# Kernel optimization log

Hardware: AMD Instinct MI355X
Metric: run time of the kernel (lower is better)

Reference implementation:

```python
import jax, jax.numpy as jnp
import numpy as np

N_HEADS = 16
ROPE_BASE = 10000.0


def _rope(x):
    # x: (B, T, H, D) -> rotary position embedding, half-split style
    T, D = x.shape[1], x.shape[-1]
    inv_freq = 1.0 / (ROPE_BASE ** (jnp.arange(0, D, 2, dtype=jnp.float32) / D))  # (D/2,)
    ang = jnp.arange(T, dtype=jnp.float32)[:, None] * inv_freq[None, :]            # (T, D/2)
    cos = jnp.cos(ang)[None, :, None, :].astype(x.dtype)
    sin = jnp.sin(ang)[None, :, None, :].astype(x.dtype)
    x1, x2 = jnp.split(x, 2, axis=-1)
    return jnp.concatenate([x1 * cos - x2 * sin, x2 * cos + x1 * sin], axis=-1)


def setup_inputs() -> dict:
    key = jax.random.key(0)
    k1, k2, k3 = jax.random.split(key, 3)
    B, T, C = 4, 2048, 2048
    init_std = 0.02
    n_layers = 24  # n_text_layers + n_vision_layers
    x = jax.random.normal(k1, (B, T, C), dtype=jnp.float32)
    Wqkv = jax.random.normal(k2, (C, 3 * C), dtype=jnp.float32) * init_std
    Wproj = jax.random.normal(k3, (C, C), dtype=jnp.float32) * (init_std * 2 * n_layers ** (-0.5))
    return {"x": x, "Wqkv": Wqkv, "Wproj": Wproj}


def reference(x, Wqkv, Wproj):
    B, T, C = x.shape
    D = C // N_HEADS
    qkv = x @ Wqkv                                  # (B, T, 3C) fused QKV projection
    q, k, v = jnp.split(qkv, 3, axis=-1)
    q = q.reshape(B, T, N_HEADS, D)
    k = k.reshape(B, T, N_HEADS, D)
    v = v.reshape(B, T, N_HEADS, D)
    q = _rope(q)
    k = _rope(k)
    y = jax.nn.dot_product_attention(q, k, v, is_causal=True)  # (B, T, H, D)
    y = y.reshape(B, T, C)
    return y @ Wproj
```

## Files before the change

### kernel.cpp

```cpp
#include <hip/hip_runtime.h>

#define BB 4
#define TT 2048
#define CC 2048
#define NHEAD 16
#define DH 128
#define MM (BB * TT)
#define N3 (3 * CC)
#define LD3 6144

typedef unsigned short u16;
typedef __attribute__((ext_vector_type(8))) short short8;
typedef __attribute__((ext_vector_type(4))) float f32x4;

__device__ __forceinline__ u16 f2bf(float f) {
  unsigned u = __float_as_uint(f);
  u += 0x7fffu + ((u >> 16) & 1u);
  return (u16)(u >> 16);
}
__device__ __forceinline__ float bf2f(u16 h) {
  return __uint_as_float(((unsigned)h) << 16);
}

__device__ __forceinline__ void gload_lds16(const void* g, void* l) {
  __builtin_amdgcn_global_load_lds((const __attribute__((address_space(1))) void*)g,
                                   (__attribute__((address_space(3))) void*)l, 16, 0, 0);
}

__device__ __forceinline__ f32x4 mfma16(short8 a, short8 b, f32x4 c) {
  return __builtin_amdgcn_mfma_f32_16x16x32_bf16(a, b, c, 0, 0, 0);
}

__global__ void convert_x_kernel(const float* __restrict__ x, u16* __restrict__ xb) {
  const int total = (MM * CC) / 4;
  const float4* xv = (const float4*)x;
  ushort4* ov = (ushort4*)xb;
  for (int i = blockIdx.x * blockDim.x + threadIdx.x; i < total; i += gridDim.x * blockDim.x) {
    float4 v = xv[i];
    ushort4 o;
    o.x = f2bf(v.x); o.y = f2bf(v.y); o.z = f2bf(v.z); o.w = f2bf(v.w);
    ov[i] = o;
  }
}

__global__ void transpose_bf16_kernel(const float* __restrict__ W, u16* __restrict__ Wt,
                                      int rows, int cols) {
  __shared__ float tile[32][33];
  const int n0 = blockIdx.x * 32, k0 = blockIdx.y * 32;
  const int tx = threadIdx.x, ty = threadIdx.y;
  #pragma unroll
  for (int i = 0; i < 4; ++i)
    tile[ty + 8 * i][tx] = W[(size_t)(k0 + ty + 8 * i) * cols + n0 + tx];
  __syncthreads();
  #pragma unroll
  for (int i = 0; i < 4; ++i)
    Wt[(size_t)(n0 + ty + 8 * i) * rows + k0 + tx] = f2bf(tile[tx][ty + 8 * i]);
}

__global__ void rope_table_kernel(float2* __restrict__ tab) {
  int idx = blockIdx.x * 256 + threadIdx.x;
  int t = idx >> 6, f = idx & 63;
  float freq = expf(-0.14391156831f * (float)f);
  float ang = (float)t * freq;
  float s, c;
  sincosf(ang, &s, &c);
  tab[idx] = make_float2(c, s);
}

__global__ void rope_apply_kernel(u16* __restrict__ qkv, const float2* __restrict__ tab) {
  int idx = blockIdx.x * 256 + threadIdx.x;
  int f8 = idx & 7;
  int h = (idx >> 3) & 15;
  int m = (idx >> 7) & 8191;
  int which = idx >> 20;
  int t = m & (TT - 1);
  u16* p = qkv + (size_t)m * LD3 + which * CC + h * DH + f8 * 8;
  short8 v1 = *(const short8*)p;
  short8 v2 = *(const short8*)(p + 64);
  const float2* cs = &tab[(t << 6) + f8 * 8];
  const float scale = which ? 1.0f : 0.08838834764831845f;
  short8 o1, o2;
  #pragma unroll
  for (int j = 0; j < 8; ++j) {
    float2 c = cs[j];
    float x1 = bf2f((u16)v1[j]), x2 = bf2f((u16)v2[j]);
    o1[j] = (short)f2bf((x1 * c.x - x2 * c.y) * scale);
    o2[j] = (short)f2bf((x2 * c.x + x1 * c.y) * scale);
  }
  *(short8*)p = o1;
  *(short8*)(p + 64) = o2;
}

#define TILE_B 32768

__device__ __forceinline__ int swz47(int x) { return x ^ (((x >> 7) & 7) << 4); }

__device__ __forceinline__ void stage_chunk(const u16* __restrict__ src, int K, int k0,
                                            char* ldsTile, int kind, int wid, int lane) {
  #pragma unroll
  for (int c = 0; c < 2; ++c) {
    int x;
    if (kind < 2) {
      x = (kind ? 8192 : 0) + c * 16384 + wid * 1024 + lane * 16;
    } else {
      int wl = wid * 2 + c;
      x = ((kind == 3) ? 4096 : 0) + (wl >> 2) * 8192 + (wl & 3) * 1024 + lane * 16;
    }
    int l = swz47(x);
    int r = l >> 7;
    int ce = (l >> 1) & 63;
    gload_lds16(src + (size_t)r * K + k0 + ce, ldsTile + (x - lane * 16));
  }
}

__global__ __launch_bounds__(512, 2) void gemm_bt_256(const u16* __restrict__ A,
                                                      const u16* __restrict__ Bt,
                                                      void* __restrict__ Cout,
                                                      int K, int ldc, int out_bf16) {
  __shared__ __align__(16) char As[2][TILE_B];
  __shared__ __align__(16) char Bs[2][TILE_B];
  const int tid = threadIdx.x;
  const int wid = tid >> 6, lane = tid & 63;
  const int l15 = lane & 15, g = lane >> 4;
  const int wr = wid >> 2, wc = wid & 3;
  const int nwg = gridDim.x * gridDim.y;
  const int orig = blockIdx.y * gridDim.x + blockIdx.x;
  const int swz = (orig & 7) * (nwg >> 3) + (orig >> 3);
  const int bx = swz % gridDim.x, by = swz / gridDim.x;
  const int row0 = by * 256, col0 = bx * 256;

  const u16* Ab = A + (size_t)row0 * K;
  const u16* Bb = Bt + (size_t)col0 * K;

  f32x4 acc[8][4];
  #pragma unroll
  for (int m = 0; m < 8; ++m)
    #pragma unroll
    for (int n = 0; n < 4; ++n) acc[m][n] = (f32x4){0.f, 0.f, 0.f, 0.f};

  const int abase = (wr * 128 + l15) * 128 + g * 16;
  const int bbase = (wc * 64 + l15) * 128 + g * 16;

  stage_chunk(Ab, K, 0, As[0], 0, wid, lane);
  stage_chunk(Bb, K, 0, Bs[0], 2, wid, lane);
  stage_chunk(Ab, K, 0, As[0], 1, wid, lane);
  stage_chunk(Bb, K, 0, Bs[0], 3, wid, lane);
  asm volatile("s_waitcnt vmcnt(0)" ::: "memory");
  __builtin_amdgcn_s_barrier();

  const int nt = K >> 6;
  short8 a[4][2], b[4][2];
  for (int t = 0; t < nt; ++t) {
    const int cur = t & 1, nxt = cur ^ 1;
    const bool hn = (t + 1) < nt;
    const int kn = (t + 1) << 6;
    const char* At = As[cur];
    const char* Btile = Bs[cur];

    if (hn) {
      stage_chunk(Ab, K, kn, As[nxt], 0, wid, lane);
      stage_chunk(Bb, K, kn, Bs[nxt], 2, wid, lane);
    }
    #pragma unroll
    for (int m = 0; m < 4; ++m)
      #pragma unroll
      for (int ks = 0; ks < 2; ++ks)
        a[m][ks] = *(const short8*)(At + swz47(abase + m * 2048 + ks * 64));
    #pragma unroll
    for (int n = 0; n < 2; ++n)
      #pragma unroll
      for (int ks = 0; ks < 2; ++ks)
        b[n][ks] = *(const short8*)(Btile + swz47(bbase + n * 2048 + ks * 64));
    __builtin_amdgcn_s_setprio(1);
    #pragma unroll
    for (int m = 0; m < 4; ++m)
      #pragma unroll
      for (int n = 0; n < 2; ++n)
        #pragma unroll
        for (int ks = 0; ks < 2; ++ks)
          acc[m][n] = mfma16(a[m][ks], b[n][ks], acc[m][n]);
    __builtin_amdgcn_s_setprio(0);

    if (hn) {
      stage_chunk(Ab, K, kn, As[nxt], 1, wid, lane);
      stage_chunk(Bb, K, kn, Bs[nxt], 3, wid, lane);
    }
    if (hn) asm volatile("s_waitcnt vmcnt(8)" ::: "memory");
    else    asm volatile("s_waitcnt vmcnt(0)" ::: "memory");
    __builtin_amdgcn_s_barrier();

    #pragma unroll
    for (int n = 2; n < 4; ++n)
      #pragma unroll
      for (int ks = 0; ks < 2; ++ks)
        b[n][ks] = *(const short8*)(Btile + swz47(bbase + n * 2048 + ks * 64));
    __builtin_amdgcn_s_setprio(1);
    #pragma unroll
    for (int m = 0; m < 4; ++m)
      #pragma unroll
      for (int n = 2; n < 4; ++n)
        #pragma unroll
        for (int ks = 0; ks < 2; ++ks)
          acc[m][n] = mfma16(a[m][ks], b[n][ks], acc[m][n]);
    __builtin_amdgcn_s_setprio(0);

    #pragma unroll
    for (int m = 0; m < 4; ++m)
      #pragma unroll
      for (int ks = 0; ks < 2; ++ks)
        a[m][ks] = *(const short8*)(At + swz47(abase + (m + 4) * 2048 + ks * 64));
    __builtin_amdgcn_s_setprio(1);
    #pragma unroll
    for (int m = 0; m < 4; ++m)
      #pragma unroll
      for (int n = 0; n < 2; ++n)
        #pragma unroll
        for (int ks = 0; ks < 2; ++ks)
          acc[m + 4][n] = mfma16(a[m][ks], b[n][ks], acc[m + 4][n]);
    __builtin_amdgcn_s_setprio(0);

    __builtin_amdgcn_s_setprio(1);
    #pragma unroll
    for (int m = 0; m < 4; ++m)
      #pragma unroll
      for (int n = 2; n < 4; ++n)
        #pragma unroll
        for (int ks = 0; ks < 2; ++ks)
          acc[m + 4][n] = mfma16(a[m][ks], b[n][ks], acc[m + 4][n]);
    __builtin_amdgcn_s_setprio(0);

    if (hn) {
      asm volatile("s_waitcnt vmcnt(4)" ::: "memory");
      __builtin_amdgcn_s_barrier();
    }
  }

  if (out_bf16) {
    u16* Cb = (u16*)Cout;
    #pragma unroll
    for (int m = 0; m < 8; ++m)
      #pragma unroll
      for (int n = 0; n < 4; ++n) {
        int row = row0 + wr * 128 + m * 16 + 4 * g;
        int col = col0 + wc * 64 + n * 16 + l15;
        #pragma unroll
        for (int j = 0; j < 4; ++j)
          Cb[(size_t)(row + j) * ldc + col] = f2bf(acc[m][n][j]);
      }
  } else {
    float* Cf = (float*)Cout;
    #pragma unroll
    for (int m = 0; m < 8; ++m)
      #pragma unroll
      for (int n = 0; n < 4; ++n) {
        int row = row0 + wr * 128 + m * 16 + 4 * g;
        int col = col0 + wc * 64 + n * 16 + l15;
        #pragma unroll
        for (int j = 0; j < 4; ++j)
          Cf[(size_t)(row + j) * ldc + col] = acc[m][n][j];
      }
  }
}

#define QBLK 128
#define KBLK 64
#define PADV 72

__global__ __launch_bounds__(256, 2) void attn_kernel(const u16* __restrict__ qkv,
                                                      u16* __restrict__ y) {
  __shared__ __align__(16) u16 Ks[2][KBLK * 128];
  __shared__ __align__(16) u16 Vt[2][DH * PADV];
  const int tid = threadIdx.x;
  const int wid = tid >> 6, lane = tid & 63;
  const int l15 = lane & 15, g = lane >> 4;
  const int b = blockIdx.y >> 4, h = blockIdx.y & 15;
  const size_t rb = (size_t)b * TT;
  const int vk0 = (tid & 15) * 4, vd0 = (tid >> 4) * 8;

  for (int half = 0; half < 2; ++half) {
    const int qt0 = (half ? (15 - (int)blockIdx.x) : (int)blockIdx.x) * QBLK;

    short8 qf[2][4];
    {
      const u16* qbase = qkv + (rb + qt0 + wid * 32 + l15) * LD3 + h * DH;
      #pragma unroll
      for (int f = 0; f < 2; ++f)
        #pragma unroll
        for (int kk = 0; kk < 4; ++kk)
          qf[f][kk] = *(const short8*)(qbase + f * 16 * LD3 + kk * 32 + g * 8);
    }

    {
      const u16* kbase = qkv + (rb)*LD3 + CC + h * DH;
      #pragma unroll
      for (int c = 0; c < 4; ++c) {
        int chunk = c * 256 + tid;
        int r = chunk >> 4, s = chunk & 15;
        gload_lds16(kbase + (size_t)r * LD3 + (size_t)((s ^ (r & 7)) * 8),
                    &Ks[0][(c * 256 + wid * 64) * 8]);
      }
      const u16* vg = qkv + (rb + vk0) * LD3 + 2 * CC + h * DH + vd0;
      short8 r0 = *(const short8*)vg;
      short8 r1 = *(const short8*)(vg + LD3);
      short8 r2 = *(const short8*)(vg + 2 * LD3);
      short8 r3 = *(const short8*)(vg + 3 * LD3);
      #pragma unroll
      for (int j = 0; j < 8; ++j) {
        ushort4 w;
        w.x = (u16)r0[j]; w.y = (u16)r1[j]; w.z = (u16)r2[j]; w.w = (u16)r3[j];
        *(ushort4*)&Vt[0][(vd0 + j) * PADV + vk0] = w;
      }
    }
    asm volatile("s_waitcnt vmcnt(0)" ::: "memory");
    __syncthreads();

    f32x4 o[2][8];
    float mrun[2][4], lrun[2][4];
    #pragma unroll
    for (int f = 0; f < 2; ++f) {
      #pragma unroll
      for (int nf = 0; nf < 8; ++nf) o[f][nf] = (f32x4){0.f, 0.f, 0.f, 0.f};
      #pragma unroll
      for (int j = 0; j < 4; ++j) { mrun[f][j] = -1e30f; lrun[f][j] = 0.f; }
    }

    const int nt = qt0 / KBLK + 2;
    for (int it = 0; it < nt; ++it) {
      const int cur = it & 1, nxt = cur ^ 1;
      const bool havenext = (it + 1) < nt;
      if (havenext) {
        const int kvn = (it + 1) * KBLK;
        const u16* kbase = qkv + (rb + kvn) * LD3 + CC + h * DH;
        #pragma unroll
        for (int c = 0; c < 4; ++c) {
          int chunk = c * 256 + tid;
          int r = chunk >> 4, s = chunk & 15;
          gload_lds16(kbase + (size_t)r * LD3 + (size_t)((s ^ (r & 7)) * 8),
                      &Ks[nxt][(c * 256 + wid * 64) * 8]);
        }
      }

      f32x4 s4[2][4];
      #pragma unroll
      for (int f = 0; f < 2; ++f)
        #pragma unroll
        for (int jf = 0; jf < 4; ++jf) s4[f][jf] = (f32x4){0.f, 0.f, 0.f, 0.f};
      #pragma unroll
      for (int jf = 0; jf < 4; ++jf) {
        int krow = jf * 16 + l15;
        #pragma unroll
        for (int kk = 0; kk < 4; ++kk) {
          short8 kf = *(const short8*)((const char*)Ks[cur] + krow * 256 +
                                       ((kk * 64 + g * 16) ^ ((l15 & 7) << 4)));
          s4[0][jf] = mfma16(qf[0][kk], kf, s4[0][jf]);
          s4[1][jf] = mfma16(qf[1][kk], kf, s4[1][jf]);
        }
      }
      if (it >= nt - 2) {
        const int kvb = it * KBLK - qt0;
        #pragma unroll
        for (int f = 0; f < 2; ++f)
          #pragma unroll
          for (int jf = 0; jf < 4; ++jf)
            #pragma unroll
            for (int j = 0; j < 4; ++j)
              if (kvb + jf * 16 + l15 > wid * 32 + f * 16 + 4 * g + j)
                s4[f][jf][j] = -1e30f;
      }
      #pragma unroll
      for (int f = 0; f < 2; ++f) {
        float rmax[4], corr[4], rsum[4];
        #pragma unroll
        for (int j = 0; j < 4; ++j)
          rmax[j] = fmaxf(fmaxf(s4[f][0][j], s4[f][1][j]), fmaxf(s4[f][2][j], s4[f][3][j]));
        #pragma unroll
        for (int j = 0; j < 4; ++j) {
          rmax[j] = fmaxf(rmax[j], __shfl_xor(rmax[j], 1, 64));
          rmax[j] = fmaxf(rmax[j], __shfl_xor(rmax[j], 2, 64));
          rmax[j] = fmaxf(rmax[j], __shfl_xor(rmax[j], 4, 64));
          rmax[j] = fmaxf(rmax[j], __shfl_xor(rmax[j], 8, 64));
        }
        #pragma unroll
        for (int j = 0; j < 4; ++j) {
          float mn = fmaxf(mrun[f][j], rmax[j]);
          corr[j] = __expf(mrun[f][j] - mn);
          mrun[f][j] = mn;
        }
        #pragma unroll
        for (int jf = 0; jf < 4; ++jf)
          #pragma unroll
          for (int j = 0; j < 4; ++j)
            s4[f][jf][j] = __expf(s4[f][jf][j] - mrun[f][j]);
        #pragma unroll
        for (int j = 0; j < 4; ++j) {
          rsum[j] = (s4[f][0][j] + s4[f][1][j]) + (s4[f][2][j] + s4[f][3][j]);
          rsum[j] += __shfl_xor(rsum[j], 1, 64);
          rsum[j] += __shfl_xor(rsum[j], 2, 64);
          rsum[j] += __shfl_xor(rsum[j], 4, 64);
          rsum[j] += __shfl_xor(rsum[j], 8, 64);
          lrun[f][j] = lrun[f][j] * corr[j] + rsum[j];
        }
        #pragma unroll
        for (int nf = 0; nf < 8; ++nf)
          #pragma unroll
          for (int j = 0; j < 4; ++j)
            o[f][nf][j] *= corr[j];
      }

      __syncthreads();
      {
        u16* Pb = (u16*)Ks[cur];
        #pragma unroll
        for (int f = 0; f < 2; ++f)
          #pragma unroll
          for (int jf = 0; jf < 4; ++jf)
            #pragma unroll
            for (int j = 0; j < 4; ++j) {
              int prow = wid * 32 + f * 16 + 4 * g + j;
              int pcol = (jf * 16 + l15) ^ (((4 * g + j) & 7) << 3);
              Pb[prow * 64 + pcol] = f2bf(s4[f][jf][j]);
            }
      }
      asm volatile("s_waitcnt lgkmcnt(0)" ::: "memory");
      __builtin_amdgcn_sched_barrier(0);
      short8 pf[2][2];
      #pragma unroll
      for (int f = 0; f < 2; ++f)
        #pragma unroll
        for (int kk = 0; kk < 2; ++kk)
          pf[f][kk] = *(const short8*)&((const u16*)Ks[cur])[
              (wid * 32 + f * 16 + l15) * 64 + ((kk * 32 + g * 8) ^ ((l15 & 7) << 3))];

      #pragma unroll
      for (int nf = 0; nf < 8; ++nf) {
        #pragma unroll
        for (int kk = 0; kk < 2; ++kk) {
          short8 vf = *(const short8*)&Vt[cur][(nf * 16 + l15) * PADV + kk * 32 + g * 8];
          o[0][nf] = mfma16(pf[0][kk], vf, o[0][nf]);
          o[1][nf] = mfma16(pf[1][kk], vf, o[1][nf]);
        }
      }

      if (havenext) {
        const int kvn = (it + 1) * KBLK;
        const u16* vg = qkv + (rb + kvn + vk0) * LD3 + 2 * CC + h * DH + vd0;
        short8 r0 = *(const short8*)vg;
        short8 r1 = *(const short8*)(vg + LD3);
        short8 r2 = *(const short8*)(vg + 2 * LD3);
        short8 r3 = *(const short8*)(vg + 3 * LD3);
        #pragma unroll
        for (int j = 0; j < 8; ++j) {
          ushort4 w;
          w.x = (u16)r0[j]; w.y = (u16)r1[j]; w.z = (u16)r2[j]; w.w = (u16)r3[j];
          *(ushort4*)&Vt[nxt][(vd0 + j) * PADV + vk0] = w;
        }
      }
      asm volatile("s_waitcnt vmcnt(0)" ::: "memory");
      __syncthreads();
    }

    #pragma unroll
    for (int f = 0; f < 2; ++f) {
      float inv[4];
      #pragma unroll
      for (int j = 0; j < 4; ++j) inv[j] = 1.0f / lrun[f][j];
      #pragma unroll
      for (int nf = 0; nf < 8; ++nf)
        #pragma unroll
        for (int j = 0; j < 4; ++j)
          y[(rb + qt0 + wid * 32 + f * 16 + 4 * g + j) * CC + h * DH + nf * 16 + l15] =
              f2bf(o[f][nf][j] * inv[j]);
    }
  }
}

extern "C" void kernel_launch(void* const* d_in, const int* in_sizes, int n_in,
                              void* d_out, int out_size, void* d_ws, size_t ws_size,
                              hipStream_t stream) {
  const float* x = (const float*)d_in[0];
  const float* Wqkv = (const float*)d_in[1];
  const float* Wproj = (const float*)d_in[2];
  char* ws = (char*)d_ws;
  u16* xb     = (u16*)(ws);
  u16* wqkvT  = (u16*)(ws + 33554432);
  u16* wprojT = (u16*)(ws + 58720256);
  u16* qkv    = (u16*)(ws + 67108864);
  u16* y      = (u16*)(ws + 167772160);
  float2* tab = (float2*)(ws + 201326592);

  convert_x_kernel<<<4096, 256, 0, stream>>>(x, xb);
  transpose_bf16_kernel<<<dim3(192, 64), dim3(32, 8), 0, stream>>>(Wqkv, wqkvT, CC, N3);
  transpose_bf16_kernel<<<dim3(64, 64), dim3(32, 8), 0, stream>>>(Wproj, wprojT, CC, CC);
  rope_table_kernel<<<512, 256, 0, stream>>>(tab);
  gemm_bt_256<<<dim3(24, 32), 512, 0, stream>>>(xb, wqkvT, (void*)qkv, CC, LD3, 1);
  rope_apply_kernel<<<8192, 256, 0, stream>>>(qkv, tab);
  attn_kernel<<<dim3(8, 64), 256, 0, stream>>>(qkv, y);
  gemm_bt_256<<<dim3(8, 32), 512, 0, stream>>>(y, wprojT, d_out, CC, CC, 0);
}
```

Measured before the change: 517.3 us.

## Restructure GEMM main loop into four barrier-separated phases with interleaved prefetch

Reorganizes the double-buffered GEMM K-loop into four compute phases. Each phase issues one quarter of the next tile's global-to-LDS loads between LDS reads and MFMA blocks, and holds B fragments in separate lo and hi registers. The aim is to spread memory traffic evenly across the iteration and overlap it with MFMA work in a ping-pong style schedule. The cost is many more workgroup barriers per iteration and more intricate vmcnt accounting, which risks stalls or subtle correctness issues.

```diff
diff --git a/kernel.cpp b/kernel.cpp
--- a/kernel.cpp
+++ b/kernel.cpp
@@ -143,24 +143,20 @@
 
   stage_chunk(Ab, K, 0, As[0], 0, wid, lane);
   stage_chunk(Bb, K, 0, Bs[0], 2, wid, lane);
+  stage_chunk(Bb, K, 0, Bs[0], 3, wid, lane);
   stage_chunk(Ab, K, 0, As[0], 1, wid, lane);
-  stage_chunk(Bb, K, 0, Bs[0], 3, wid, lane);
   asm volatile("s_waitcnt vmcnt(0)" ::: "memory");
   __builtin_amdgcn_s_barrier();
 
   const int nt = K >> 6;
-  short8 a[4][2], b[4][2];
-  for (int t = 0; t < nt; ++t) {
-    const int cur = t & 1, nxt = cur ^ 1;
-    const bool hn = (t + 1) < nt;
-    const int kn = (t + 1) << 6;
+  short8 a[4][2], blo[2][2], bhi[2][2];
+  for (int kt = 0; kt < nt; ++kt) {
+    const int cur = kt & 1, nx = cur ^ 1;
+    const bool hn = (kt + 1) < nt;
+    const int kn = (kt + 1) << 6;
     const char* At = As[cur];
-    const char* Btile = Bs[cur];
-
-    if (hn) {
-      stage_chunk(Ab, K, kn, As[nxt], 0, wid, lane);
-      stage_chunk(Bb, K, kn, Bs[nxt], 2, wid, lane);
-    }
+    const char* Btl = Bs[cur];
+
     #pragma unroll
     for (int m = 0; m < 4; ++m)
       #pragma unroll
@@ -170,7 +166,9 @@
     for (int n = 0; n < 2; ++n)
       #pragma unroll
       for (int ks = 0; ks < 2; ++ks)
-        b[n][ks] = *(const short8*)(Btile + swz47(bbase + n * 2048 + ks * 64));
+        blo[n][ks] = *(const short8*)(Btl + swz47(bbase + n * 2048 + ks * 64));
+    if (hn) stage_chunk(Ab, K, kn, As[nx], 0, wid, lane);
+    __builtin_amdgcn_s_barrier();
     __builtin_amdgcn_s_setprio(1);
     #pragma unroll
     for (int m = 0; m < 4; ++m)
@@ -178,37 +176,39 @@
       for (int n = 0; n < 2; ++n)
         #pragma unroll
         for (int ks = 0; ks < 2; ++ks)
-          acc[m][n] = mfma16(a[m][ks], b[n][ks], acc[m][n]);
+          acc[m][n] = mfma16(a[m][ks], blo[n][ks], acc[m][n]);
     __builtin_amdgcn_s_setprio(0);
-
-    if (hn) {
-      stage_chunk(Ab, K, kn, As[nxt], 1, wid, lane);
-      stage_chunk(Bb, K, kn, Bs[nxt], 3, wid, lane);
-    }
-    if (hn) asm volatile("s_waitcnt vmcnt(8)" ::: "memory");
+    if (hn) asm volatile("s_waitcnt vmcnt(4)" ::: "memory");
+    else    asm volatile("s_waitcnt vmcnt(2)" ::: "memory");
+    __builtin_amdgcn_s_barrier();
+
+    #pragma unroll
+    for (int n = 0; n < 2; ++n)
+      #pragma unroll
+      for (int ks = 0; ks < 2; ++ks)
+        bhi[n][ks] = *(const short8*)(Btl + swz47(bbase + (n + 2) * 2048 + ks * 64));
+    if (hn) stage_chunk(Bb, K, kn, Bs[nx], 2, wid, lane);
+    __builtin_amdgcn_s_barrier();
+    __builtin_amdgcn_s_setprio(1);
+    #pragma unroll
+    for (int m = 0; m < 4; ++m)
+      #pragma unroll
+      for (int n = 0; n < 2; ++n)
+        #pragma unroll
+        for (int ks = 0; ks < 2; ++ks)
+          acc[m][n + 2] = mfma16(a[m][ks], bhi[n][ks], acc[m][n + 2]);
+    __builtin_amdgcn_s_setprio(0);
+    if (hn) asm volatile("s_waitcnt vmcnt(4)" ::: "memory");
     else    asm volatile("s_waitcnt vmcnt(0)" ::: "memory");
     __builtin_amdgcn_s_barrier();
-
-    #pragma unroll
-    for (int n = 2; n < 4; ++n)
-      #pragma unroll
-      for (int ks = 0; ks < 2; ++ks)
-        b[n][ks] = *(const short8*)(Btile + swz47(bbase + n * 2048 + ks * 64));
-    __builtin_amdgcn_s_setprio(1);
-    #pragma unroll
-    for (int m = 0; m < 4; ++m)
-      #pragma unroll
-      for (int n = 2; n < 4; ++n)
-        #pragma unroll
-        for (int ks = 0; ks < 2; ++ks)
-          acc[m][n] = mfma16(a[m][ks], b[n][ks], acc[m][n]);
-    __builtin_amdgcn_s_setprio(0);
 
     #pragma unroll
     for (int m = 0; m < 4; ++m)
       #pragma unroll
       for (int ks = 0; ks < 2; ++ks)
         a[m][ks] = *(const short8*)(At + swz47(abase + (m + 4) * 2048 + ks * 64));
+    if (hn) stage_chunk(Bb, K, kn, Bs[nx], 3, wid, lane);
+    __builtin_amdgcn_s_barrier();
     __builtin_amdgcn_s_setprio(1);
     #pragma unroll
     for (int m = 0; m < 4; ++m)
@@ -216,23 +216,24 @@
       for (int n = 0; n < 2; ++n)
         #pragma unroll
         for (int ks = 0; ks < 2; ++ks)
-          acc[m + 4][n] = mfma16(a[m][ks], b[n][ks], acc[m + 4][n]);
+          acc[m + 4][n] = mfma16(a[m][ks], blo[n][ks], acc[m + 4][n]);
     __builtin_amdgcn_s_setprio(0);
-
+    if (hn) asm volatile("s_waitcnt vmcnt(4)" ::: "memory");
+    __builtin_amdgcn_s_barrier();
+
+    if (hn) stage_chunk(Ab, K, kn, As[nx], 1, wid, lane);
+    __builtin_amdgcn_s_barrier();
     __builtin_amdgcn_s_setprio(1);
     #pragma unroll
     for (int m = 0; m < 4; ++m)
       #pragma unroll
-      for (int n = 2; n < 4; ++n)
+      for (int n = 0; n < 2; ++n)
         #pragma unroll
         for (int ks = 0; ks < 2; ++ks)
-          acc[m + 4][n] = mfma16(a[m][ks], b[n][ks], acc[m + 4][n]);
+          acc[m + 4][n + 2] = mfma16(a[m][ks], bhi[n][ks], acc[m + 4][n + 2]);
     __builtin_amdgcn_s_setprio(0);
-
-    if (hn) {
-      asm volatile("s_waitcnt vmcnt(4)" ::: "memory");
-      __builtin_amdgcn_s_barrier();
-    }
+    if (hn) asm volatile("s_waitcnt vmcnt(4)" ::: "memory");
+    __builtin_amdgcn_s_barrier();
   }
 
   if (out_bf16) {
```

Result: faster. 498.0 us (-3.7%).
